# Kernel tuning notes

Measured on AMD Instinct MI355X. Metric: run time of the kernel, lower is better.

Reference implementation:

```python
import jax, jax.numpy as jnp
import numpy as np

K = 1  # top-k experts per image


def cv_squared(v):
    # squared coefficient of variation; torch .var() is unbiased -> ddof=1
    eps = 1e-10
    m = v.mean()
    var = v.var(ddof=1)
    return jnp.where(jnp.abs(m) < eps, jnp.zeros((), v.dtype), var / (m * m + eps))


def setup_inputs() -> dict:
    key = jax.random.key(0)
    k0, k1, k2, k3 = jax.random.split(key, 4)
    B, H, W, C, E, HID = 64, 32, 32, 512, 5, 2048
    x = jax.random.normal(k0, (B, H, W, C), jnp.float32)
    # xavier-uniform-like scale for the gate
    gate_scale = float(np.sqrt(6.0 / (C + E)))
    w_gate = jax.random.uniform(k1, (C, E), jnp.float32, -gate_scale, gate_scale)
    W1 = jax.random.normal(k2, (E, C, HID), jnp.float32) * 0.02
    b1 = jnp.zeros((E, HID), jnp.float32)
    W2 = jax.random.normal(k3, (E, HID, C), jnp.float32) * 0.02
    b2 = jnp.zeros((E, C), jnp.float32)
    return {"x": x, "w_gate": w_gate, "W1": W1, "b1": b1, "W2": W2, "b2": b2}


def reference(x, w_gate, W1, b1, W2, b2):
    B, H, W_, C = x.shape
    E = w_gate.shape[1]
    xt = x.reshape(B, H * W_, C)              # [B, T, C] tokens
    xg = x.mean(axis=(1, 2))                  # [B, C] per-image gating feature

    # eval-mode noisy_top_k_gating (no noise): clean logits, clamp, top-k softmax
    logits = jnp.clip(xg @ w_gate, -50.0, 50.0)          # [B, E]
    top_logits, top_idx = jax.lax.top_k(logits, min(K + 1, E))
    tk_logits = top_logits[:, :K]
    tk_idx = top_idx[:, :K]                               # [B, K]
    tk_gates = jax.nn.softmax(tk_logits, axis=1)          # [B, K]
    gates = jnp.zeros_like(logits).at[jnp.arange(B)[:, None], tk_idx].set(tk_gates)

    importance = gates.sum(axis=0)                        # [E]
    load = (gates > 0).sum(axis=0).astype(jnp.float32)    # [E]
    loss = jnp.clip(cv_squared(importance) + cv_squared(load), 0.0, 1000.0)

    # dispatch: every token of image b goes through its top-K experts
    y = jnp.zeros_like(xt)
    for ki in range(K):
        idx = tk_idx[:, ki]                               # [B] expert id per image
        h = jnp.einsum('btd,bdh->bth', xt, W1[idx]) + b1[idx][:, None, :]
        h = jax.nn.gelu(h, approximate=False)             # torch nn.GELU default (erf)
        o = jnp.einsum('bth,bhd->btd', h, W2[idx]) + b2[idx][:, None, :]
        y = y + tk_gates[:, ki][:, None, None] * o

    return y.reshape(B, H, W_, C), loss
```

## Files before the change

kernel.cpp:

```cpp
#include <hip/hip_runtime.h>
#include <hip/hip_bf16.h>
#include <math.h>

typedef __attribute__((ext_vector_type(4))) float f4_t;
typedef __attribute__((ext_vector_type(8))) short s8_t;

constexpr int Bc = 64;
constexpr int Tc = 1024;
constexpr int Cc = 512;
constexpr int Ec = 5;
constexpr int HIDc = 2048;

__device__ __forceinline__ void async_copy16(const void* gsrc, void* ldst) {
  __builtin_amdgcn_global_load_lds(
      (const __attribute__((address_space(1))) unsigned int*)gsrc,
      (__attribute__((address_space(3))) unsigned int*)ldst, 16, 0, 0);
}

__device__ __forceinline__ float gelu_f(float v) {
  float v2 = v * v;
  float z = v * (1.5957691216f + 0.0713548162f * v2);
  float e = __expf(z);
  float r = __frcp_rn(1.0f + e);
  return v - v * r;
}


__global__ void k_prep(const float* __restrict__ x, ushort* __restrict__ xbf,
                       float* __restrict__ part) {
  int b = blockIdx.x, p = blockIdx.y, tid = threadIdx.x;
  const float4* xp = (const float4*)(x + ((size_t)b * Tc + (size_t)p * 128) * Cc);
  ushort4* op = (ushort4*)(xbf + ((size_t)b * Tc + (size_t)p * 128) * Cc);
  int c4 = tid & 127, r0 = tid >> 7;
  float4 s = {0.f, 0.f, 0.f, 0.f};
  for (int r = r0; r < 128; r += 2) {
    float4 v = xp[(size_t)r * 128 + c4];
    s.x += v.x; s.y += v.y; s.z += v.z; s.w += v.w;
    union { __hip_bfloat16 h[4]; ushort4 u; } cv;
    cv.h[0] = __float2bfloat16(v.x);
    cv.h[1] = __float2bfloat16(v.y);
    cv.h[2] = __float2bfloat16(v.z);
    cv.h[3] = __float2bfloat16(v.w);
    op[(size_t)r * 128 + c4] = cv.u;
  }
  __shared__ float4 sh[128];
  if (r0) sh[c4] = s;
  __syncthreads();
  if (!r0) {
    float4 o = sh[c4];
    s.x += o.x; s.y += o.y; s.z += o.z; s.w += o.w;
    ((float4*)part)[(size_t)(b * 8 + p) * 128 + c4] = s;
  }
}

__global__ void k_partial(const float* __restrict__ x, float* __restrict__ part) {
  int b = blockIdx.x, p = blockIdx.y, tid = threadIdx.x;
  const float* xp = x + ((size_t)b * Tc + (size_t)p * 128) * Cc;
  float s0 = 0.f, s1 = 0.f;
  for (int t = 0; t < 128; ++t) {
    s0 += xp[(size_t)t * Cc + tid];
    s1 += xp[(size_t)t * Cc + tid + 256];
  }
  part[(size_t)(b * 8 + p) * Cc + tid] = s0;
  part[(size_t)(b * 8 + p) * Cc + tid + 256] = s1;
}

__global__ void k_cvt_x(const float* __restrict__ src, ushort* __restrict__ dst, int n4) {
  int i = blockIdx.x * blockDim.x + threadIdx.x;
  int stride = gridDim.x * blockDim.x;
  const float4* s4 = (const float4*)src;
  ushort4* d4 = (ushort4*)dst;
  for (; i < n4; i += stride) {
    float4 v = s4[i];
    union { __hip_bfloat16 h[4]; ushort4 u; } cv;
    cv.h[0] = __float2bfloat16(v.x);
    cv.h[1] = __float2bfloat16(v.y);
    cv.h[2] = __float2bfloat16(v.z);
    cv.h[3] = __float2bfloat16(v.w);
    d4[i] = cv.u;
  }
}

__global__ void k_xg_logits(const float* __restrict__ part, const float* __restrict__ wg,
                            float* __restrict__ logits) {
  __shared__ float xg[Cc];
  __shared__ float red[Ec][4];
  int b = blockIdx.x, tid = threadIdx.x;
  for (int c = tid; c < Cc; c += 256) {
    float s = 0.f;
#pragma unroll
    for (int p = 0; p < 8; ++p) s += part[(size_t)(b * 8 + p) * Cc + c];
    xg[c] = s * (1.0f / 1024.0f);
  }
  __syncthreads();
  float le[Ec] = {0.f, 0.f, 0.f, 0.f, 0.f};
  for (int c = tid; c < Cc; c += 256) {
    float v = xg[c];
#pragma unroll
    for (int e = 0; e < Ec; ++e) le[e] += v * wg[c * Ec + e];
  }
#pragma unroll
  for (int e = 0; e < Ec; ++e) {
    float v = le[e];
#pragma unroll
    for (int off = 32; off > 0; off >>= 1) v += __shfl_down(v, off);
    if ((tid & 63) == 0) red[e][tid >> 6] = v;
  }
  __syncthreads();
  if (tid < Ec) {
    float v = red[tid][0] + red[tid][1] + red[tid][2] + red[tid][3];
    v = fminf(fmaxf(v, -50.f), 50.f);
    logits[b * Ec + tid] = v;
  }
}

__global__ void k_gate(const float* __restrict__ logits, int* __restrict__ idx,
                       float* __restrict__ loss_out) {
  __shared__ int cnt[Ec];
  int tid = threadIdx.x;
  if (tid < Ec) cnt[tid] = 0;
  __syncthreads();
  if (tid < Bc) {
    const float* lb = logits + tid * Ec;
    int best = 0;
    float bv = lb[0];
#pragma unroll
    for (int e = 1; e < Ec; ++e) {
      float v = lb[e];
      if (v > bv) { bv = v; best = e; }
    }
    idx[tid] = best;
    atomicAdd(&cnt[best], 1);
  }
  __syncthreads();
  if (tid == 0) {
    const float mean = (float)Bc / (float)Ec;
    float var = 0.f;
#pragma unroll
    for (int e = 0; e < Ec; ++e) {
      float d = (float)cnt[e] - mean;
      var += d * d;
    }
    var *= (1.0f / (Ec - 1));
    float loss = 2.f * (var / (mean * mean + 1e-10f));
    loss = fminf(fmaxf(loss, 0.f), 1000.f);
    *loss_out = loss;
  }
}

__global__ void k_transpose_cvt(const float* __restrict__ src, __hip_bfloat16* __restrict__ dst,
                                int K, int N) {
  __shared__ float tile[32][33];
  int e = blockIdx.z;
  int kb = blockIdx.y * 32, nb = blockIdx.x * 32;
  const float* s = src + (size_t)e * K * N;
  __hip_bfloat16* d = dst + (size_t)e * K * N;
  int lx = threadIdx.x & 31, ly = threadIdx.x >> 5;
#pragma unroll
  for (int r = 0; r < 4; ++r) {
    int k = kb + ly + r * 8;
    tile[ly + r * 8][lx] = s[(size_t)k * N + nb + lx];
  }
  __syncthreads();
#pragma unroll
  for (int r = 0; r < 4; ++r) {
    int n = nb + ly + r * 8;
    d[(size_t)n * K + kb + lx] = __float2bfloat16(tile[lx][ly + r * 8]);
  }
}


#define GEMM_PRELUDE(KDIM)                                               \
  int tid = threadIdx.x, l = tid & 63, w = tid >> 6;                     \
  int wr = w >> 2, wc = w & 3;                                           \
  const short* gA[4];                                                    \
  const short* gB[4];                                                    \
  int loff[4];                                                           \
  _Pragma("unroll")                                                      \
  for (int i = 0; i < 4; ++i) {                                          \
    int sp = i * 512 + tid;                                              \
    int r = sp >> 3;                                                     \
    int c8 = ((sp & 7) ^ (r & 7)) << 3;                                  \
    gA[i] = Ab + (size_t)r * (KDIM) + c8;                                \
    gB[i] = Bb + (size_t)r * (KDIM) + c8;                                \
    loff[i] = sp * 16;                                                   \
  }                                                                      \
  int abase = (wr * 128 + (l & 15)) * 128;                               \
  int bbase = (wc * 64 + (l & 15)) * 128;                                \
  int s0 = (((l >> 4)) ^ (l & 7)) << 4;                                  \
  int s1 = (((l >> 4) + 4) ^ (l & 7)) << 4;

#define STAGE_A_HALF(buf, h, kt)                                         \
  {                                                                      \
    char* d_ = (char*)&lds[buf][0][0];                                   \
    int k0_ = (kt) * 64;                                                 \
    async_copy16(gA[2 * (h)] + k0_, d_ + loff[2 * (h)]);                 \
    async_copy16(gA[2 * (h) + 1] + k0_, d_ + loff[2 * (h) + 1]);         \
  }
#define STAGE_B_HALF(buf, h, kt)                                         \
  {                                                                      \
    char* d_ = (char*)&lds[buf][1][0];                                   \
    int k0_ = (kt) * 64;                                                 \
    async_copy16(gB[2 * (h)] + k0_, d_ + loff[2 * (h)]);                 \
    async_copy16(gB[2 * (h) + 1] + k0_, d_ + loff[2 * (h) + 1]);         \
  }

#define PH8(q, tt, NTv)                                                      \
  {                                                                          \
    const char* As_ = (const char*)&lds[(tt) & 1][0][0];                     \
    const char* Bs_ = (const char*)&lds[(tt) & 1][1][0];                     \
    if ((q) == 0) {                                                          \
      _Pragma("unroll")                                                      \
      for (int fn = 0; fn < 4; ++fn) {                                       \
        bfr[fn * 2 + 0] = *(const s8_t*)(Bs_ + bbase + fn * 2048 + s0);      \
        bfr[fn * 2 + 1] = *(const s8_t*)(Bs_ + bbase + fn * 2048 + s1);      \
      }                                                                      \
    }                                                                        \
    afr[0] = *(const s8_t*)(As_ + abase + ((q) * 2 + 0) * 2048 + s0);        \
    afr[1] = *(const s8_t*)(As_ + abase + ((q) * 2 + 0) * 2048 + s1);        \
    afr[2] = *(const s8_t*)(As_ + abase + ((q) * 2 + 1) * 2048 + s0);        \
    afr[3] = *(const s8_t*)(As_ + abase + ((q) * 2 + 1) * 2048 + s1);        \
    if ((q) == 0 && (tt) + 1 < (NTv)) STAGE_A_HALF(((tt) + 1) & 1, 0, (tt) + 1) \
    if ((q) == 1 && (tt) + 1 < (NTv)) STAGE_A_HALF(((tt) + 1) & 1, 1, (tt) + 1) \
    if ((q) == 2 && (tt) + 2 < (NTv)) STAGE_B_HALF((tt) & 1, 0, (tt) + 2)    \
    if ((q) == 3 && (tt) + 2 < (NTv)) STAGE_B_HALF((tt) & 1, 1, (tt) + 2)    \
    __builtin_amdgcn_s_barrier();                                            \
    asm volatile("s_waitcnt lgkmcnt(0)" ::: "memory");                       \
    __builtin_amdgcn_sched_barrier(0);                                       \
    __builtin_amdgcn_s_setprio(1);                                           \
    _Pragma("unroll")                                                        \
    for (int kk = 0; kk < 2; ++kk)                                           \
      _Pragma("unroll")                                                      \
      for (int j = 0; j < 2; ++j)                                            \
        _Pragma("unroll")                                                    \
        for (int fn = 0; fn < 4; ++fn)                                       \
          acc[(q) * 2 + j][fn] = __builtin_amdgcn_mfma_f32_16x16x32_bf16(    \
              afr[j * 2 + kk], bfr[fn * 2 + kk], acc[(q) * 2 + j][fn], 0, 0, 0); \
    __builtin_amdgcn_s_setprio(0);                                           \
    if ((q) == 3) {                                                          \
      if ((tt) + 2 < (NTv)) {                                                \
        asm volatile("s_waitcnt vmcnt(4)" ::: "memory");                     \
      } else if ((tt) + 1 < (NTv)) {                                         \
        asm volatile("s_waitcnt vmcnt(0)" ::: "memory");                     \
      }                                                                      \
    }                                                                        \
    __builtin_amdgcn_s_barrier();                                            \
    asm volatile("" ::: "memory");                                           \
  }

#define KLOOP8(NTv)                                                      \
  s8_t bfr[8], afr[4];                                                   \
  STAGE_B_HALF(0, 0, 0)                                                  \
  STAGE_B_HALF(0, 1, 0)                                                  \
  STAGE_A_HALF(0, 0, 0)                                                  \
  STAGE_A_HALF(0, 1, 0)                                                  \
  STAGE_B_HALF(1, 0, 1)                                                  \
  STAGE_B_HALF(1, 1, 1)                                                  \
  asm volatile("s_waitcnt vmcnt(4)" ::: "memory");                       \
  __builtin_amdgcn_s_barrier();                                          \
  asm volatile("" ::: "memory");                                         \
  _Pragma("unroll 2")                                                    \
  for (int t = 0; t < (NTv); ++t) {                                      \
    PH8(0, t, NTv)                                                       \
    PH8(1, t, NTv)                                                       \
    PH8(2, t, NTv)                                                       \
    PH8(3, t, NTv)                                                       \
  }

__global__ __launch_bounds__(512, 2) void k_gemm1(
    const __hip_bfloat16* __restrict__ xbf, const __hip_bfloat16* __restrict__ w1t,
    const float* __restrict__ b1, const int* __restrict__ idx, int b0, int nz,
    __hip_bfloat16* __restrict__ h) {
  constexpr int K = Cc;
  constexpr int N = HIDc;
  constexpr int NT = K / 64;
  constexpr int NBX = N / 256, NBY = Tc / 256;
  __shared__ short lds[2][2][256 * 64];

  int nwg = NBX * NBY * nz;
  int cpx = nwg >> 3;
  int lg = (blockIdx.x & 7) * cpx + (blockIdx.x >> 3);
  int bx = lg % NBX, by = (lg / NBX) % NBY, bz = lg / (NBX * NBY);

  int e = idx[b0 + bz];
  int m0 = by * 256, n0 = bx * 256;
  const short* Ab = (const short*)xbf + ((size_t)bz * Tc + m0) * K;
  const short* Bb = (const short*)w1t + ((size_t)e * N + n0) * K;

  GEMM_PRELUDE(K)
  f4_t acc[8][4] = {};
  KLOOP8(NT)

  __syncthreads();
  short* chunk = &lds[0][0][0] + w * (64 * 72);
  const float* bias = b1 + (size_t)e * N;
  short* hb = (short*)(h + (size_t)bz * Tc * N);
  int cc2 = (l & 7) * 8;
#pragma unroll
  for (int p = 0; p < 2; ++p) {
#pragma unroll
    for (int fn = 0; fn < 4; ++fn) {
      float bv = bias[n0 + wc * 64 + fn * 16 + (l & 15)];
#pragma unroll
      for (int fm = 0; fm < 4; ++fm) {
        int rl = fm * 16 + ((l >> 4) << 2);
#pragma unroll
        for (int j = 0; j < 4; ++j) {
          float v = gelu_f(acc[p * 4 + fm][fn][j] + bv);
          chunk[(rl + j) * 72 + fn * 16 + (l & 15)] =
              (short)__bfloat16_as_ushort(__float2bfloat16(v));
        }
      }
    }
#pragma unroll
    for (int q = 0; q < 8; ++q) {
      int rr = q * 8 + (l >> 3);
      s8_t v = *(const s8_t*)(chunk + rr * 72 + cc2);
      *(s8_t*)(hb + (size_t)(m0 + wr * 128 + p * 64 + rr) * N + n0 + wc * 64 + cc2) = v;
    }
    asm volatile("s_waitcnt lgkmcnt(0)" ::: "memory");
  }
}

__global__ __launch_bounds__(512, 2) void k_gemm2(
    const __hip_bfloat16* __restrict__ h, const __hip_bfloat16* __restrict__ w2t,
    const float* __restrict__ b2, const int* __restrict__ idx, int b0, int nz,
    float* __restrict__ out) {
  constexpr int K = HIDc;
  constexpr int N = Cc;
  constexpr int NT = K / 64;
  constexpr int NBX = N / 256, NBY = Tc / 256;
  __shared__ short lds[2][2][256 * 64];

  int nwg = NBX * NBY * nz;
  int cpx = nwg >> 3;
  int lg = (blockIdx.x & 7) * cpx + (blockIdx.x >> 3);
  int bx = lg % NBX, by = (lg / NBX) % NBY, bz = lg / (NBX * NBY);

  int e = idx[b0 + bz];
  int m0 = by * 256, n0 = bx * 256;
  const short* Ab = (const short*)h + ((size_t)bz * Tc + m0) * K;
  const short* Bb = (const short*)w2t + ((size_t)e * N + n0) * K;

  GEMM_PRELUDE(K)
  f4_t acc[8][4] = {};
  KLOOP8(NT)

  float* ob = out + (size_t)(b0 + bz) * Tc * N;
  const float* bias = b2 + (size_t)e * N;
#pragma unroll
  for (int fn = 0; fn < 4; ++fn) {
    int col = n0 + wc * 64 + fn * 16 + (l & 15);
    float bv = bias[col];
#pragma unroll
    for (int fm = 0; fm < 8; ++fm) {
      int rbase = m0 + wr * 128 + fm * 16 + ((l >> 4) << 2);
#pragma unroll
      for (int j = 0; j < 4; ++j) {
        ob[(size_t)(rbase + j) * N + col] = acc[fm][fn][j] + bv;
      }
    }
  }
}

extern "C" void kernel_launch(void* const* d_in, const int* in_sizes, int n_in,
                              void* d_out, int out_size, void* d_ws, size_t ws_size,
                              hipStream_t stream) {
  const float* x  = (const float*)d_in[0];
  const float* wg = (const float*)d_in[1];
  const float* W1 = (const float*)d_in[2];
  const float* b1 = (const float*)d_in[3];
  const float* W2 = (const float*)d_in[4];
  const float* b2 = (const float*)d_in[5];
  float* out = (float*)d_out;

  char* ws = (char*)d_ws;
  size_t off = 0;
  float* part = (float*)(ws + off); off += (size_t)Bc * 8 * Cc * 4;
  float* logits = (float*)(ws + off); off += (size_t)Bc * Ec * 4;
  int* idx = (int*)(ws + off); off += (size_t)Bc * 4;
  off = (off + 255) & ~(size_t)255;
  __hip_bfloat16* w1t = (__hip_bfloat16*)(ws + off); off += (size_t)Ec * HIDc * Cc * 2;
  __hip_bfloat16* w2t = (__hip_bfloat16*)(ws + off); off += (size_t)Ec * HIDc * Cc * 2;
  size_t dynoff = (off + 255) & ~(size_t)255;

  const size_t x_all = (size_t)Bc * Tc * Cc * 2;
  const size_t x_per_b = (size_t)Tc * Cc * 2;
  const size_t h_per_b = (size_t)Tc * HIDc * 2;

  k_transpose_cvt<<<dim3(HIDc / 32, Cc / 32, Ec), 256, 0, stream>>>(W1, w1t, Cc, HIDc);
  k_transpose_cvt<<<dim3(Cc / 32, HIDc / 32, Ec), 256, 0, stream>>>(W2, w2t, HIDc, Cc);

  if (ws_size >= dynoff + x_all + h_per_b) {
    __hip_bfloat16* xbf = (__hip_bfloat16*)(ws + dynoff);
    __hip_bfloat16* hbf = (__hip_bfloat16*)(ws + dynoff + x_all);
    int cb = (int)((ws_size - dynoff - x_all) / h_per_b);
    if (cb > Bc) cb = Bc;

    k_prep<<<dim3(Bc, 8), 256, 0, stream>>>(x, (ushort*)xbf, part);
    k_xg_logits<<<dim3(Bc), 256, 0, stream>>>(part, wg, logits);
    k_gate<<<dim3(1), 256, 0, stream>>>(logits, idx, out + ((size_t)out_size - 1));

    for (int b0 = 0; b0 < Bc; b0 += cb) {
      int c = (Bc - b0) < cb ? (Bc - b0) : cb;
      const __hip_bfloat16* xc = xbf + (size_t)b0 * Tc * Cc;
      k_gemm1<<<dim3((HIDc / 256) * (Tc / 256) * c), 512, 0, stream>>>(
          xc, w1t, b1, idx, b0, c, hbf);
      k_gemm2<<<dim3((Cc / 256) * (Tc / 256) * c), 512, 0, stream>>>(
          hbf, w2t, b2, idx, b0, c, out);
    }
  } else {
    size_t avail = ws_size > dynoff ? ws_size - dynoff : 0;
    int cb = (int)(avail / (x_per_b + h_per_b));
    if (cb > Bc) cb = Bc;
    if (cb < 1) cb = 1;
    __hip_bfloat16* xbf = (__hip_bfloat16*)(ws + dynoff);
    __hip_bfloat16* hbf = (__hip_bfloat16*)(ws + dynoff + (size_t)cb * x_per_b);

    k_partial<<<dim3(Bc, 8), 256, 0, stream>>>(x, part);
    k_xg_logits<<<dim3(Bc), 256, 0, stream>>>(part, wg, logits);
    k_gate<<<dim3(1), 256, 0, stream>>>(logits, idx, out + ((size_t)out_size - 1));

    for (int b0 = 0; b0 < Bc; b0 += cb) {
      int c = (Bc - b0) < cb ? (Bc - b0) : cb;
      int n4 = c * (Tc * Cc / 4);
      k_cvt_x<<<dim3(1024), 256, 0, stream>>>(x + (size_t)b0 * Tc * Cc, (ushort*)xbf, n4);
      k_gemm1<<<dim3((HIDc / 256) * (Tc / 256) * c), 512, 0, stream>>>(
          xbf, w1t, b1, idx, b0, c, hbf);
      k_gemm2<<<dim3((Cc / 256) * (Tc / 256) * c), 512, 0, stream>>>(
          hbf, w2t, b2, idx, b0, c, out);
    }
  }
}
```

Measured before the change: 436.8 us.

## Software-pipeline LDS fragment reads with double-buffered A fragments in GEMM loop

Restructures the GEMM inner loop so the LDS reads for the next quad's A fragments, and for the next tile's B fragments, are issued right after the current quad's MFMAs. Two alternating A-fragment register sets let those reads overlap with matrix math. This removes the barrier-then-`lgkmcnt(0)` stall that used to sit in front of every MFMA group. In exchange it uses more registers, and the next-tile reads at the last quad now run after only a per-wave `vmcnt` wait but before the workgroup barrier, so they may see another wave's copy that has not finished.

Result: no change. 438.0 us (+0.3%).

```diff
diff --git a/kernel.cpp b/kernel.cpp
--- a/kernel.cpp
+++ b/kernel.cpp
@@ -205,28 +205,27 @@
     async_copy16(gB[2 * (h) + 1] + k0_, d_ + loff[2 * (h) + 1]);         \
   }
 
-#define PH8(q, tt, NTv)                                                      \
+#define READ_QUAD(AFR, bufp, qq)                                         \
+  {                                                                      \
+    const char* Aq_ = (const char*)&lds[bufp][0][0];                     \
+    AFR[0] = *(const s8_t*)(Aq_ + abase + ((qq) * 2 + 0) * 2048 + s0);   \
+    AFR[1] = *(const s8_t*)(Aq_ + abase + ((qq) * 2 + 0) * 2048 + s1);   \
+    AFR[2] = *(const s8_t*)(Aq_ + abase + ((qq) * 2 + 1) * 2048 + s0);   \
+    AFR[3] = *(const s8_t*)(Aq_ + abase + ((qq) * 2 + 1) * 2048 + s1);   \
+  }
+
+#define READ_BFR(bufp)                                                   \
+  {                                                                      \
+    const char* Bq_ = (const char*)&lds[bufp][1][0];                     \
+    _Pragma("unroll")                                                    \
+    for (int fn = 0; fn < 4; ++fn) {                                     \
+      bfr[fn * 2 + 0] = *(const s8_t*)(Bq_ + bbase + fn * 2048 + s0);    \
+      bfr[fn * 2 + 1] = *(const s8_t*)(Bq_ + bbase + fn * 2048 + s1);    \
+    }                                                                    \
+  }
+
+#define PH_PIPE(q, tt, NTv, ACUR, ANXT)                                      \
   {                                                                          \
-    const char* As_ = (const char*)&lds[(tt) & 1][0][0];                     \
-    const char* Bs_ = (const char*)&lds[(tt) & 1][1][0];                     \
-    if ((q) == 0) {                                                          \
-      _Pragma("unroll")                                                      \
-      for (int fn = 0; fn < 4; ++fn) {                                       \
-        bfr[fn * 2 + 0] = *(const s8_t*)(Bs_ + bbase + fn * 2048 + s0);      \
-        bfr[fn * 2 + 1] = *(const s8_t*)(Bs_ + bbase + fn * 2048 + s1);      \
-      }                                                                      \
-    }                                                                        \
-    afr[0] = *(const s8_t*)(As_ + abase + ((q) * 2 + 0) * 2048 + s0);        \
-    afr[1] = *(const s8_t*)(As_ + abase + ((q) * 2 + 0) * 2048 + s1);        \
-    afr[2] = *(const s8_t*)(As_ + abase + ((q) * 2 + 1) * 2048 + s0);        \
-    afr[3] = *(const s8_t*)(As_ + abase + ((q) * 2 + 1) * 2048 + s1);        \
-    if ((q) == 0 && (tt) + 1 < (NTv)) STAGE_A_HALF(((tt) + 1) & 1, 0, (tt) + 1) \
-    if ((q) == 1 && (tt) + 1 < (NTv)) STAGE_A_HALF(((tt) + 1) & 1, 1, (tt) + 1) \
-    if ((q) == 2 && (tt) + 2 < (NTv)) STAGE_B_HALF((tt) & 1, 0, (tt) + 2)    \
-    if ((q) == 3 && (tt) + 2 < (NTv)) STAGE_B_HALF((tt) & 1, 1, (tt) + 2)    \
-    __builtin_amdgcn_s_barrier();                                            \
-    asm volatile("s_waitcnt lgkmcnt(0)" ::: "memory");                       \
-    __builtin_amdgcn_sched_barrier(0);                                       \
     __builtin_amdgcn_s_setprio(1);                                           \
     _Pragma("unroll")                                                        \
     for (int kk = 0; kk < 2; ++kk)                                           \
@@ -235,21 +234,32 @@
         _Pragma("unroll")                                                    \
         for (int fn = 0; fn < 4; ++fn)                                       \
           acc[(q) * 2 + j][fn] = __builtin_amdgcn_mfma_f32_16x16x32_bf16(    \
-              afr[j * 2 + kk], bfr[fn * 2 + kk], acc[(q) * 2 + j][fn], 0, 0, 0); \
+              ACUR[j * 2 + kk], bfr[fn * 2 + kk], acc[(q) * 2 + j][fn], 0, 0, 0); \
     __builtin_amdgcn_s_setprio(0);                                           \
-    if ((q) == 3) {                                                          \
+    if ((q) == 0 && (tt) + 1 < (NTv)) STAGE_A_HALF(((tt) + 1) & 1, 0, (tt) + 1) \
+    if ((q) == 1 && (tt) + 1 < (NTv)) STAGE_A_HALF(((tt) + 1) & 1, 1, (tt) + 1) \
+    if ((q) == 2 && (tt) + 2 < (NTv)) STAGE_B_HALF((tt) & 1, 0, (tt) + 2)    \
+    if ((q) == 3 && (tt) + 2 < (NTv)) STAGE_B_HALF((tt) & 1, 1, (tt) + 2)    \
+    if ((q) < 3) {                                                           \
+      READ_QUAD(ANXT, (tt) & 1, (q) + 1)                                     \
+    } else {                                                                 \
       if ((tt) + 2 < (NTv)) {                                                \
         asm volatile("s_waitcnt vmcnt(4)" ::: "memory");                     \
       } else if ((tt) + 1 < (NTv)) {                                         \
         asm volatile("s_waitcnt vmcnt(0)" ::: "memory");                     \
       }                                                                      \
+      if ((tt) + 1 < (NTv)) {                                                \
+        READ_BFR(((tt) + 1) & 1)                                             \
+        READ_QUAD(ANXT, ((tt) + 1) & 1, 0)                                   \
+        asm volatile("s_waitcnt lgkmcnt(0)" ::: "memory");                   \
+      }                                                                      \
     }                                                                        \
     __builtin_amdgcn_s_barrier();                                            \
     asm volatile("" ::: "memory");                                           \
   }
 
 #define KLOOP8(NTv)                                                      \
-  s8_t bfr[8], afr[4];                                                   \
+  s8_t bfr[8], afrA[4], afrB[4];                                         \
   STAGE_B_HALF(0, 0, 0)                                                  \
   STAGE_B_HALF(0, 1, 0)                                                  \
   STAGE_A_HALF(0, 0, 0)                                                  \
@@ -259,12 +269,14 @@
   asm volatile("s_waitcnt vmcnt(4)" ::: "memory");                       \
   __builtin_amdgcn_s_barrier();                                          \
   asm volatile("" ::: "memory");                                         \
+  READ_BFR(0)                                                            \
+  READ_QUAD(afrA, 0, 0)                                                  \
   _Pragma("unroll 2")                                                    \
   for (int t = 0; t < (NTv); ++t) {                                      \
-    PH8(0, t, NTv)                                                       \
-    PH8(1, t, NTv)                                                       \
-    PH8(2, t, NTv)                                                       \
-    PH8(3, t, NTv)                                                       \
+    PH_PIPE(0, t, NTv, afrA, afrB)                                       \
+    PH_PIPE(1, t, NTv, afrB, afrA)                                       \
+    PH_PIPE(2, t, NTv, afrA, afrB)                                       \
+    PH_PIPE(3, t, NTv, afrB, afrA)                                       \
   }
 
 __global__ __launch_bounds__(512, 2) void k_gemm1(
@@ -289,7 +301,7 @@
 
   GEMM_PRELUDE(K)
   f4_t acc[8][4] = {};
-  KLOOP8(NT)
+  { KLOOP8(NT) }
 
   __syncthreads();
   short* chunk = &lds[0][0][0] + w * (64 * 72);
@@ -344,7 +356,7 @@
 
   GEMM_PRELUDE(K)
   f4_t acc[8][4] = {};
-  KLOOP8(NT)
+  { KLOOP8(NT) }
 
   float* ob = out + (size_t)(b0 + bz) * Tc * N;
   const float* bias = b2 + (size_t)e * N;
```
